# Kernel tuning notes

Hardware: AMD Instinct MI355X
Metric: run time of the kernel (lower is better)

## Reference

```python
import jax, jax.numpy as jnp
import numpy as np

N_USERS = 100000
N_ITEMS = 100000
N_BICLIQUES = 50000
NNZ = 2000000
D = 64


def setup_inputs() -> dict:
    key = jax.random.key(0)
    k1, k2, k3, k4, k5, k6 = jax.random.split(key, 6)
    return {
        "user_emb": jax.random.normal(k1, (N_USERS, D), dtype=jnp.float32),
        "item_emb": jax.random.normal(k2, (N_ITEMS, D), dtype=jnp.float32),
        "hv_rows": jax.random.randint(k3, (NNZ,), 0, N_BICLIQUES, dtype=jnp.int32),
        "hv_cols": jax.random.randint(k4, (NNZ,), 0, N_ITEMS, dtype=jnp.int32),
        "hv_vals": jnp.ones((NNZ,), dtype=jnp.float32),
        "hu_rows": jax.random.randint(k5, (NNZ,), 0, N_USERS, dtype=jnp.int32),
        "hu_cols": jax.random.randint(k6, (NNZ,), 0, N_BICLIQUES, dtype=jnp.int32),
        "hu_vals": jnp.ones((NNZ,), dtype=jnp.float32),
        "n_bicliques": N_BICLIQUES,
        "n_users": N_USERS,
    }


def _spmm_mean(rows, cols, vals, dense, num_segments):
    # out[r] = (sum_{e: rows[e]==r} vals[e] * dense[cols[e]]) / max(degree[r], treat 0 as 1)
    # degree[r] = sum of vals on row r (matches torch.sparse.sum(dim=1)).
    num = jax.ops.segment_sum(vals[:, None] * dense[cols], rows, num_segments=num_segments)
    deg = jax.ops.segment_sum(vals, rows, num_segments=num_segments)
    deg = jnp.where(deg == 0, 1.0, deg)[:, None]
    return num / deg


def reference(user_emb, item_emb, hv_rows, hv_cols, hv_vals, hu_rows, hu_cols, hu_vals, n_bicliques, n_users):
    # Hop 1: biclique features = row-mean of item embeddings via H_v [n_bicliques, n_items]
    biclique_features = _spmm_mean(hv_rows, hv_cols, hv_vals, item_emb, n_bicliques)
    # Hop 2: user local view = row-mean of biclique features via H_u [n_users, n_bicliques]
    user_local_view = _spmm_mean(hu_rows, hu_cols, hu_vals, biclique_features, n_users)
    return user_local_view
```

## Files before the change

kernel.cpp:

```cpp
#include <hip/hip_runtime.h>
#include <hip/hip_fp16.h>


#define DIM 64
#define CAP 2944
#define CHUNK 16384
#define P1B 512
#define EPT (CHUNK / P1B)
#define NBIN 782
#define SH1 6
#define SH2 7
#define PITCH (NBIN + 1)

__global__ __launch_bounds__(P1B) void pass1_kernel(
    const int* __restrict__ rows1, const int* __restrict__ cols1,
    const float* __restrict__ vals1, int nnz1, int nc1, int ncb,
    const int* __restrict__ rows2, const int* __restrict__ cols2,
    const float* __restrict__ vals2, int nnz2,
    int2* __restrict__ st1, int* __restrict__ ofs1,
    int2* __restrict__ st2, int* __restrict__ ofs2,
    const float4* __restrict__ cvt_in, int2* __restrict__ cvt_out, int n4) {
    __shared__ int2 sorted[CHUNK];
    __shared__ int hist[NBIN];
    __shared__ int excl[NBIN];
    __shared__ int cur[NBIN];
    __shared__ int wtot[9];
    const int t = threadIdx.x;

    if ((int)blockIdx.x >= ncb) {
        int i0 = (blockIdx.x - ncb) * (P1B * 8) + t;
        #pragma unroll
        for (int k = 0; k < 8; ++k) {
            int i = i0 + k * P1B;
            if (i < n4) {
                float4 x = cvt_in[i];
                __half2 h0 = __float22half2_rn(make_float2(x.x, x.y));
                __half2 h1 = __float22half2_rn(make_float2(x.z, x.w));
                int2 pk;
                pk.x = *(int*)&h0;
                pk.y = *(int*)&h1;
                cvt_out[i] = pk;
            }
        }
        return;
    }
    const int* rows; const int* cols; const float* vals;
    int nnz, shift, chunk_id;
    int2* st; int* ofs;
    if ((int)blockIdx.x < nc1) {
        rows = rows1; cols = cols1; vals = vals1; nnz = nnz1;
        shift = SH1; chunk_id = blockIdx.x; st = st1; ofs = ofs1;
    } else {
        rows = rows2; cols = cols2; vals = vals2; nnz = nnz2;
        shift = SH2; chunk_id = blockIdx.x - nc1; st = st2; ofs = ofs2;
    }
    for (int i = t; i < NBIN; i += P1B) hist[i] = 0;
    __syncthreads();
    int begin = chunk_id * CHUNK;

    int r[EPT]; int c[EPT]; float v[EPT];
    #pragma unroll
    for (int k = 0; k < EPT; ++k) {
        int idx = begin + k * P1B + t;
        bool ok = idx < nnz;
        r[k] = ok ? rows[idx] : -1;
        c[k] = ok ? cols[idx] : 0;
        v[k] = ok ? vals[idx] : 0.0f;
        if (ok) atomicAdd(&hist[r[k] >> shift], 1);
    }
    __syncthreads();
    int b0 = 2 * t;
    int h0 = 0, pv = 0;
    if (b0 < NBIN) {
        h0 = hist[b0];
        pv = h0 + ((b0 + 1 < NBIN) ? hist[b0 + 1] : 0);
    }
    int x = pv;
    #pragma unroll
    for (int o = 1; o < 64; o <<= 1) {
        int n = __shfl_up(x, o);
        if ((t & 63) >= o) x += n;
    }
    if ((t & 63) == 63) wtot[t >> 6] = x;
    __syncthreads();
    if (t == 0) {
        int acc = 0;
        #pragma unroll
        for (int w = 0; w < 8; ++w) { int tmp = wtot[w]; wtot[w] = acc; acc += tmp; }
        wtot[8] = acc;
    }
    __syncthreads();
    int ex = x - pv + wtot[t >> 6];
    if (b0 < NBIN) {
        excl[b0] = ex; cur[b0] = ex;
        if (b0 + 1 < NBIN) { excl[b0 + 1] = ex + h0; cur[b0 + 1] = ex + h0; }
    }
    const int chunk_len = wtot[8];
    __syncthreads();
    #pragma unroll
    for (int k = 0; k < EPT; ++k) {
        if (r[k] >= 0) {
            int bb = r[k] >> shift;
            int pos = atomicAdd(&cur[bb], 1);
            int key = ((r[k] - (bb << shift)) << 17) | c[k];
            sorted[pos] = make_int2(key, __float_as_int(v[k]));
        }
    }
    __syncthreads();
    size_t cbase = (size_t)chunk_id * CHUNK;
    for (int i = t; i < chunk_len; i += P1B) st[cbase + i] = sorted[i];
    int* orow = ofs + (size_t)chunk_id * PITCH;
    for (int i = t; i <= NBIN; i += P1B)
        orow[i] = (i < NBIN) ? excl[i] : chunk_len;
}

template <int RPB, bool DST_HALF>
__global__ __launch_bounds__(P1B) void sort_gather_kernel(
    const int2* __restrict__ st, const int* __restrict__ ofs, int nc,
    const __half* __restrict__ src, void* __restrict__ dstv, int n_rows) {
    __shared__ int2 concat[CAP];
    __shared__ int2 edges[CAP];
    __shared__ int dstA[P1B + 1];
    __shared__ int sofs[P1B];
    __shared__ int excl[RPB];
    __shared__ int cur[RPB];
    __shared__ int wtot[9];
    const int b = blockIdx.x;
    const int t = threadIdx.x;
    const int row0 = b * RPB;

    int so = 0, len = 0;
    if (t < nc) {
        const int* rowp = ofs + (size_t)t * PITCH + b;
        so  = rowp[0];
        len = rowp[1] - rowp[0];
    }
    if (t < RPB) cur[t] = 0;
    int x = len;
    #pragma unroll
    for (int o = 1; o < 64; o <<= 1) {
        int n = __shfl_up(x, o);
        if ((t & 63) >= o) x += n;
    }
    if ((t & 63) == 63) wtot[t >> 6] = x;
    __syncthreads();
    if (t == 0) {
        int acc = 0;
        #pragma unroll
        for (int w = 0; w < 8; ++w) { int tmp = wtot[w]; wtot[w] = acc; acc += tmp; }
        wtot[8] = acc;
    }
    __syncthreads();
    dstA[t] = x - len + wtot[t >> 6];
    sofs[t] = so;
    if (t == 0) dstA[P1B] = wtot[8];
    const int cnt_b = min(wtot[8], CAP);
    __syncthreads();

    {
        int g  = t >> 2;
        int lg = t & 3;
        for (int cs = g; cs < nc; cs += 128) {
            int d0 = dstA[cs];
            int L  = dstA[cs + 1] - d0;
            const int2* sp = st + (size_t)cs * CHUNK + sofs[cs];
            for (int i = lg; i < L; i += 4) {
                int p = d0 + i;
                if (p < CAP) {
                    int2 ed = sp[i];
                    concat[p] = ed;
                    atomicAdd(&cur[ed.x >> 17], 1);
                }
            }
        }
    }
    __syncthreads();
    if (t < RPB) {
        int cc = cur[t];
        int x2 = cc;
        #pragma unroll
        for (int o = 1; o < 64; o <<= 1) {
            int n = __shfl_up(x2, o);
            if ((t & 63) >= o) x2 += n;
        }
        excl[t] = x2 - cc;
        if (RPB > 64 && (t & 63) == 63) wtot[t >> 6] = x2;
    }
    __syncthreads();
    if (t < RPB) {
        int e = excl[t];
        if (RPB > 64 && t >= 64) e += wtot[0];
        excl[t] = e;
        cur[t]  = e;
    }
    __syncthreads();
    for (int i = t; i < cnt_b; i += P1B) {
        int2 ed = concat[i];
        int pos = atomicAdd(&cur[ed.x >> 17], 1);
        edges[pos] = make_int2(ed.x & 0x1FFFF, ed.y);
    }
    __syncthreads();

    const int wave = t >> 6;
    const int lane = t & 63;
    const int sub = lane >> 4;
    const int ld  = lane & 15;
    const __half* srcl = src + ld * 4;
    for (int rl = wave; rl < RPB; rl += 8) {
        int row = row0 + rl;
        if (row >= n_rows) break;
        int start = excl[rl];
        int end   = cur[rl];
        float ax = 0.f, ay = 0.f, az = 0.f, aw = 0.f, vsum = 0.f;
        for (int i = start + sub; i < end; i += 16) {
            int lim = end - 1;
            int j1 = min(i + 4,  lim);
            int j2 = min(i + 8,  lim);
            int j3 = min(i + 12, lim);
            int2 e0 = edges[i];
            int2 e1 = edges[j1];
            int2 e2 = edges[j2];
            int2 e3 = edges[j3];
            float v0 = __int_as_float(e0.y);
            float v1 = (i + 4  < end) ? __int_as_float(e1.y) : 0.f;
            float v2 = (i + 8  < end) ? __int_as_float(e2.y) : 0.f;
            float v3 = (i + 12 < end) ? __int_as_float(e3.y) : 0.f;
            int2 r0 = *(const int2*)(srcl + (e0.x << 6));
            int2 r1 = *(const int2*)(srcl + (e1.x << 6));
            int2 r2 = *(const int2*)(srcl + (e2.x << 6));
            int2 r3 = *(const int2*)(srcl + (e3.x << 6));
            float2 a0 = __half22float2(*(__half2*)&r0.x);
            float2 b0 = __half22float2(*(__half2*)&r0.y);
            float2 a1 = __half22float2(*(__half2*)&r1.x);
            float2 b1 = __half22float2(*(__half2*)&r1.y);
            float2 a2 = __half22float2(*(__half2*)&r2.x);
            float2 b2 = __half22float2(*(__half2*)&r2.y);
            float2 a3 = __half22float2(*(__half2*)&r3.x);
            float2 b3 = __half22float2(*(__half2*)&r3.y);
            ax += v0 * a0.x + v1 * a1.x + v2 * a2.x + v3 * a3.x;
            ay += v0 * a0.y + v1 * a1.y + v2 * a2.y + v3 * a3.y;
            az += v0 * b0.x + v1 * b1.x + v2 * b2.x + v3 * b3.x;
            aw += v0 * b0.y + v1 * b1.y + v2 * b2.y + v3 * b3.y;
            vsum += (v0 + v1) + (v2 + v3);
        }
        #pragma unroll
        for (int off = 16; off <= 32; off <<= 1) {
            ax += __shfl_xor(ax, off);
            ay += __shfl_xor(ay, off);
            az += __shfl_xor(az, off);
            aw += __shfl_xor(aw, off);
            vsum += __shfl_xor(vsum, off);
        }
        float d = (vsum == 0.0f) ? 1.0f : vsum;
        if (sub == 0) {
            float inv = 1.0f / d;
            if (DST_HALF) {
                __half* dst = (__half*)dstv;
                __half2 o0 = __float22half2_rn(make_float2(ax * inv, ay * inv));
                __half2 o1 = __float22half2_rn(make_float2(az * inv, aw * inv));
                int2 pk;
                pk.x = *(int*)&o0;
                pk.y = *(int*)&o1;
                *(int2*)(dst + row * DIM + ld * 4) = pk;
            } else {
                float* dst = (float*)dstv;
                float4 o = make_float4(ax * inv, ay * inv, az * inv, aw * inv);
                *(float4*)(dst + row * DIM + ld * 4) = o;
            }
        }
    }
}

extern "C" void kernel_launch(void* const* d_in, const int* in_sizes, int n_in,
                              void* d_out, int out_size, void* d_ws, size_t ws_size,
                              hipStream_t stream) {
    const float* item_emb = (const float*)d_in[1];
    const int*   hv_rows  = (const int*)d_in[2];
    const int*   hv_cols  = (const int*)d_in[3];
    const float* hv_vals  = (const float*)d_in[4];
    const int*   hu_rows  = (const int*)d_in[5];
    const int*   hu_cols  = (const int*)d_in[6];
    const float* hu_vals  = (const float*)d_in[7];

    const int nnz1 = in_sizes[2];
    const int nnz2 = in_sizes[5];
    const int n_items = in_sizes[1] / DIM;
    const int n_b  = 50000;
    const int n_u  = out_size / DIM;

    float* out = (float*)d_out;

    int nc1 = (nnz1 + CHUNK - 1) / CHUNK;
    int nc2 = (nnz2 + CHUNK - 1) / CHUNK;

    char* p = (char*)d_ws;
    __half* item_h = (__half*)p; p += (size_t)n_items * DIM * sizeof(__half);
    __half* bf_h   = (__half*)p; p += (size_t)n_b * DIM * sizeof(__half);
    int2*  st1     = (int2*)p;   p += (size_t)nc1 * CHUNK * sizeof(int2);
    int2*  st2     = (int2*)p;   p += (size_t)nc2 * CHUNK * sizeof(int2);
    int*   ofs1    = (int*)p;    p += (size_t)nc1 * PITCH * sizeof(int);
    int*   ofs2    = (int*)p;    p += (size_t)nc2 * PITCH * sizeof(int);

    int n4 = n_items * DIM / 4;
    int ncb = nc1 + nc2;
    int ncv = (n4 + P1B * 8 - 1) / (P1B * 8);

    pass1_kernel<<<ncb + ncv, P1B, 0, stream>>>(
        hv_rows, hv_cols, hv_vals, nnz1, nc1, ncb,
        hu_rows, hu_cols, hu_vals, nnz2,
        st1, ofs1, st2, ofs2,
        (const float4*)item_emb, (int2*)item_h, n4);

    sort_gather_kernel<64, true><<<NBIN, P1B, 0, stream>>>(
        st1, ofs1, nc1, item_h, bf_h, n_b);
    sort_gather_kernel<128, false><<<NBIN, P1B, 0, stream>>>(
        st2, ofs2, nc2, bf_h, out, n_u);
}
```

Measured before the change: 263.2 us.

## Split each bin across two blocks and read chunk edges twice from global

Each sort_gather bin is now processed by two blocks, each owning half of the bin's rows. The shared-memory concat staging buffer and the block-wide scan are removed. Instead each block scans the chunk segments twice, once to count and once to scatter its own rows' edges directly into a smaller edges buffer. This doubles the grid and cuts LDS per block, which should raise occupancy, at the cost of reading every bin's edges from global memory twice per block and four times per bin.

```diff
diff --git a/kernel.cpp b/kernel.cpp
--- a/kernel.cpp
+++ b/kernel.cpp
@@ -3,7 +3,7 @@
 
 
 #define DIM 64
-#define CAP 2944
+#define CAPH 1792
 #define CHUNK 16384
 #define P1B 512
 #define EPT (CHUNK / P1B)
@@ -118,86 +118,62 @@
 __global__ __launch_bounds__(P1B) void sort_gather_kernel(
     const int2* __restrict__ st, const int* __restrict__ ofs, int nc,
     const __half* __restrict__ src, void* __restrict__ dstv, int n_rows) {
-    __shared__ int2 concat[CAP];
-    __shared__ int2 edges[CAP];
-    __shared__ int dstA[P1B + 1];
-    __shared__ int sofs[P1B];
+    __shared__ int2 edges[CAPH];
+    __shared__ int sofs[136];
+    __shared__ int slen[136];
     __shared__ int excl[RPB];
     __shared__ int cur[RPB];
-    __shared__ int wtot[9];
     const int b = blockIdx.x;
+    const int parent = b >> 1;
+    const int half = b & 1;
     const int t = threadIdx.x;
-    const int row0 = b * RPB;
-
-    int so = 0, len = 0;
+    const int row0 = parent * (2 * RPB) + half * RPB;
+    constexpr int LOG2 = (RPB == 32) ? 5 : 6;
+
+    if (t < RPB) cur[t] = 0;
     if (t < nc) {
-        const int* rowp = ofs + (size_t)t * PITCH + b;
-        so  = rowp[0];
-        len = rowp[1] - rowp[0];
-    }
-    if (t < RPB) cur[t] = 0;
-    int x = len;
-    #pragma unroll
-    for (int o = 1; o < 64; o <<= 1) {
-        int n = __shfl_up(x, o);
-        if ((t & 63) >= o) x += n;
-    }
-    if ((t & 63) == 63) wtot[t >> 6] = x;
-    __syncthreads();
-    if (t == 0) {
-        int acc = 0;
-        #pragma unroll
-        for (int w = 0; w < 8; ++w) { int tmp = wtot[w]; wtot[w] = acc; acc += tmp; }
-        wtot[8] = acc;
-    }
-    __syncthreads();
-    dstA[t] = x - len + wtot[t >> 6];
-    sofs[t] = so;
-    if (t == 0) dstA[P1B] = wtot[8];
-    const int cnt_b = min(wtot[8], CAP);
-    __syncthreads();
-
-    {
-        int g  = t >> 2;
-        int lg = t & 3;
-        for (int cs = g; cs < nc; cs += 128) {
-            int d0 = dstA[cs];
-            int L  = dstA[cs + 1] - d0;
-            const int2* sp = st + (size_t)cs * CHUNK + sofs[cs];
-            for (int i = lg; i < L; i += 4) {
-                int p = d0 + i;
-                if (p < CAP) {
-                    int2 ed = sp[i];
-                    concat[p] = ed;
-                    atomicAdd(&cur[ed.x >> 17], 1);
-                }
-            }
+        const int* rowp = ofs + (size_t)t * PITCH + parent;
+        sofs[t] = rowp[0];
+        slen[t] = rowp[1] - rowp[0];
+    }
+    __syncthreads();
+
+    const int g  = t >> 2;
+    const int lg = t & 3;
+    for (int cs = g; cs < nc; cs += 128) {
+        const int2* sp = st + (size_t)cs * CHUNK + sofs[cs];
+        int L = slen[cs];
+        for (int i = lg; i < L; i += 4) {
+            int rb = sp[i].x >> 17;
+            if ((rb >> LOG2) == half)
+                atomicAdd(&cur[rb & (RPB - 1)], 1);
         }
     }
     __syncthreads();
     if (t < RPB) {
         int cc = cur[t];
-        int x2 = cc;
-        #pragma unroll
-        for (int o = 1; o < 64; o <<= 1) {
-            int n = __shfl_up(x2, o);
-            if ((t & 63) >= o) x2 += n;
-        }
-        excl[t] = x2 - cc;
-        if (RPB > 64 && (t & 63) == 63) wtot[t >> 6] = x2;
-    }
-    __syncthreads();
-    if (t < RPB) {
-        int e = excl[t];
-        if (RPB > 64 && t >= 64) e += wtot[0];
-        excl[t] = e;
-        cur[t]  = e;
-    }
-    __syncthreads();
-    for (int i = t; i < cnt_b; i += P1B) {
-        int2 ed = concat[i];
-        int pos = atomicAdd(&cur[ed.x >> 17], 1);
-        edges[pos] = make_int2(ed.x & 0x1FFFF, ed.y);
+        int x = cc;
+        #pragma unroll
+        for (int o = 1; o < RPB; o <<= 1) {
+            int n = __shfl_up(x, o);
+            if ((t & 63) >= o) x += n;
+        }
+        excl[t] = x - cc;
+        cur[t]  = x - cc;
+    }
+    __syncthreads();
+    for (int cs = g; cs < nc; cs += 128) {
+        const int2* sp = st + (size_t)cs * CHUNK + sofs[cs];
+        int L = slen[cs];
+        for (int i = lg; i < L; i += 4) {
+            int2 ed = sp[i];
+            int rb = ed.x >> 17;
+            if ((rb >> LOG2) == half) {
+                int pos = atomicAdd(&cur[rb & (RPB - 1)], 1);
+                if (pos < CAPH)
+                    edges[pos] = make_int2(ed.x & 0x1FFFF, ed.y);
+            }
+        }
     }
     __syncthreads();
 
@@ -209,8 +185,8 @@
     for (int rl = wave; rl < RPB; rl += 8) {
         int row = row0 + rl;
         if (row >= n_rows) break;
-        int start = excl[rl];
-        int end   = cur[rl];
+        int start = min(excl[rl], CAPH);
+        int end   = min(cur[rl],  CAPH);
         float ax = 0.f, ay = 0.f, az = 0.f, aw = 0.f, vsum = 0.f;
         for (int i = start + sub; i < end; i += 16) {
             int lim = end - 1;
@@ -311,8 +287,8 @@
         st1, ofs1, st2, ofs2,
         (const float4*)item_emb, (int2*)item_h, n4);
 
-    sort_gather_kernel<64, true><<<NBIN, P1B, 0, stream>>>(
+    sort_gather_kernel<32, true><<<2 * NBIN, P1B, 0, stream>>>(
         st1, ofs1, nc1, item_h, bf_h, n_b);
-    sort_gather_kernel<128, false><<<NBIN, P1B, 0, stream>>>(
+    sort_gather_kernel<64, false><<<2 * NBIN, P1B, 0, stream>>>(
         st2, ofs2, nc2, bf_h, out, n_u);
 }
```

Result: no change. 263.9 us (+0.3%).
